# Kernel optimization log

Hardware: AMD Instinct MI355X
Metric: run time of the kernel (lower is better)

## Reference

```python
import jax, jax.numpy as jnp
import numpy as np

B, CIN, COUT = 16, 32, 64
T, H, W = 20, 32, 32
KT, KH, KW = 3, 3, 3
EPS = 1e-8
SURR_SCALE = 10.0  # SuperSpike surrogate slope


@jax.custom_vjp
def spike(x):
    # forward: heaviside; backward: SuperSpike surrogate gradient
    return (x > 0).astype(x.dtype)

def _spike_fwd(x):
    return (x > 0).astype(x.dtype), x

def _spike_bwd(x, g):
    return (g / (SURR_SCALE * jnp.abs(x) + 1.0) ** 2,)

spike.defvjp(_spike_fwd, _spike_bwd)


def _conv3d(x, w, pad, groups):
    return jax.lax.conv_general_dilated(
        x, w, window_strides=(1, 1, 1),
        padding=[(pad[0], pad[0]), (pad[1], pad[1]), (pad[2], pad[2])],
        rhs_dilation=(1, 1, 1),
        dimension_numbers=('NCDHW', 'OIDHW', 'NCDHW'),
        feature_group_count=groups)


def setup_inputs() -> dict:
    key = jax.random.key(0)
    k0, k1, k2 = jax.random.split(key, 3)
    w_init_mean, w_init_std = 0.05, 0.05
    w_mean = np.sqrt(w_init_mean)
    w_std = np.sqrt(np.sqrt(w_init_mean ** 2 + (w_init_std * np.sqrt(1.0 / (CIN * KT * KH * KW))) ** 2) - w_init_mean)
    x = jax.random.normal(k0, (B, CIN, T, H, W), dtype=jnp.float32)
    w_dw = w_mean + w_std * jax.random.normal(k1, (CIN, 1, KT, KH, KW), dtype=jnp.float32)
    w_pw = w_mean + w_std * jax.random.normal(k2, (COUT, CIN, 1, 1, 1), dtype=jnp.float32)
    beta = jnp.full((1,), 0.9, dtype=jnp.float32)  # one_per_layer, constant init, clamped [0,1]
    b = jnp.ones((COUT,), dtype=jnp.float32)       # constant init 1.0, clamped >= 0
    return {'x': x, 'w_dw': w_dw, 'w_pw': w_pw, 'beta': beta, 'b': b}


def reference(x, w_dw, w_pw, beta, b):
    pad = (1, 1, 1)  # ceil((3-1)*1/2) per dim; same padding also (faithfully) used for the 1x1x1 conv
    conv_x = _conv3d(x, w_dw, pad, CIN)[:, :, :, :H, :W]          # depthwise, crop to input_shape
    conv_x = _conv3d(conv_x, w_pw, pad, 1)[:, :, :, :H, :W]        # pointwise (time grows T -> T+2)
    nb_steps = conv_x.shape[2]

    # effective full kernel = depthwise * pointwise (broadcast over kernel dims)
    w_tmp = jnp.broadcast_to(jnp.transpose(w_dw, (1, 0, 2, 3, 4)), (COUT, CIN, KT, KH, KW)) * w_pw
    d = jnp.einsum('abcde,fbcde->af', w_tmp, w_tmp)                # lateral inhibition matrix [COUT, COUT]
    norm = (w_tmp ** 2).sum((1, 2, 3, 4))                          # [COUT]
    inv_norm = 1.0 / (norm + EPS)

    def step(carry, inp):
        mem, spk = carry
        rst = jnp.einsum('abcd,be->aecd', spk, d)                  # lateral reset
        mem = (mem - rst) * beta + inp * (1.0 - beta)              # leaky soft-reset update
        mthr = mem * inv_norm[None, :, None, None] - b[None, :, None, None]
        spk = spike(mthr)
        return (mem, spk), spk

    conv_t = jnp.moveaxis(conv_x, 2, 0)                            # [nb_steps, B, COUT, H, W]
    zeros = jnp.zeros((B, COUT, H, W), dtype=x.dtype)
    _, spks = jax.lax.scan(step, (zeros, zeros), conv_t)
    spk_rec = jnp.moveaxis(spks, 0, 2)                             # [B, COUT, nb_steps, H, W]

    loss = 0.5 * (spk_rec ** 2).mean()                             # 'squared'
    spk_spread_loss = spk_rec.sum((0, 1, 3, 4)).max() / (B * COUT * H * W)  # 'max'
    return spk_rec, loss, spk_spread_loss
```

## Files before the change

kernel.cpp:

```cpp
#include <hip/hip_runtime.h>

#define BB_   16
#define CIN_  32
#define COUT_ 64
#define TT_   20
#define NSTEP 22
#define NPIX  1024
#define HW_   32

typedef float f32x16 __attribute__((ext_vector_type(16)));

#define N_DWOUT 10485760ULL
#define N_DW2   10485760ULL
#define OFF_DWOUT 0ULL
#define OFF_DW2   (OFF_DWOUT + N_DWOUT)
#define OFF_D     (OFF_DW2 + N_DW2)
#define OFF_INVN  (OFF_D + 4096ULL)
#define OFF_CNT   (OFF_INVN + 64ULL)
#define WS_FLOATS (OFF_CNT + 32ULL)

__global__ __launch_bounds__(128)
void k_depthwise(const float* __restrict__ x, const float* __restrict__ wdw,
                 float* __restrict__ dwout) {
    const int blk = blockIdx.x;
    const int t4 = blk & 3;
    const int ci = (blk >> 2) & 31;
    const int b  = blk >> 7;
    const int tid = threadIdx.x;
    __shared__ float pl[3][34][35];

    float w[27];
#pragma unroll
    for (int k = 0; k < 27; ++k) w[k] = wdw[ci * 27 + k];

    for (int i = tid; i < 3 * 34 * 35; i += 128) (&pl[0][0][0])[i] = 0.f;
    __syncthreads();

    const float* xb = x + (size_t)(b * 32 + ci) * TT_ * NPIX;
    const int lr = tid >> 2;
    const int lc = (tid & 3) * 8;

    auto load_plane = [&](int p, int slot) {
        const float* s = xb + (size_t)p * NPIX + lr * 32 + lc;
        float4 v0 = *(const float4*)s;
        float4 v1 = *(const float4*)(s + 4);
        float* d = &pl[slot][1 + lr][1 + lc];
        d[0] = v0.x; d[1] = v0.y; d[2] = v0.z; d[3] = v0.w;
        d[4] = v1.x; d[5] = v1.y; d[6] = v1.z; d[7] = v1.w;
    };
    auto zero_plane = [&](int slot) {
        float* d = &pl[slot][1 + lr][1 + lc];
#pragma unroll
        for (int j = 0; j < 8; ++j) d[j] = 0.f;
    };

    const int T0 = t4 * 5;
    if (T0 > 0) load_plane(T0 - 1, (T0 - 1) % 3);
    load_plane(T0, T0 % 3);

    const int hd = lr, wd0 = lc;
    const float* base = &pl[0][0][0];

    for (int t = T0; t < T0 + 5; ++t) {
        __syncthreads();
        const int pnext = t + 1;
        if (pnext < TT_) load_plane(pnext, pnext % 3);
        else             zero_plane(pnext % 3);
        __syncthreads();

        const int sm1 = (t + 2) % 3, s0 = t % 3, sp1 = (t + 1) % 3;
        float acc[8] = {0.f,0.f,0.f,0.f,0.f,0.f,0.f,0.f};
#pragma unroll
        for (int kt = 0; kt < 3; ++kt) {
            const int slot = (kt == 0) ? sm1 : (kt == 1) ? s0 : sp1;
            const float* Pp = base + slot * (34 * 35);
#pragma unroll
            for (int kh = 0; kh < 3; ++kh) {
                const float* row = Pp + (hd + kh) * 35 + wd0;
                float r[10];
#pragma unroll
                for (int m = 0; m < 10; ++m) r[m] = row[m];
#pragma unroll
                for (int kw = 0; kw < 3; ++kw) {
                    const float wv = w[(kt * 3 + kh) * 3 + kw];
#pragma unroll
                    for (int j = 0; j < 8; ++j) acc[j] = fmaf(wv, r[j + kw], acc[j]);
                }
            }
        }
        float* dst = dwout + ((size_t)(b * 32 + ci) * TT_ + t) * NPIX + hd * 32 + wd0;
        *(float4*)dst       = make_float4(acc[0], acc[1], acc[2], acc[3]);
        *(float4*)(dst + 4) = make_float4(acc[4], acc[5], acc[6], acc[7]);
    }
}

__global__ __launch_bounds__(256)
void k_dmat(const float* __restrict__ wdw, const float* __restrict__ wpw,
            float* __restrict__ dmat, float* __restrict__ invn,
            unsigned* __restrict__ gcnt) {
    __shared__ double S[32];
    const int tid = threadIdx.x;
    if (tid < NSTEP) gcnt[tid] = 0u;
    if (tid < 32) {
        double s = 0.0;
        for (int k = 0; k < 27; ++k) { double v = (double)wdw[tid * 27 + k]; s += v * v; }
        S[tid] = s;
    }
    __syncthreads();
    for (int e = tid; e < 4096; e += 256) {
        const int a = e >> 6, f = e & 63;
        double acc = 0.0;
        for (int ci = 0; ci < 32; ++ci)
            acc += (double)wpw[a * 32 + ci] * (double)wpw[f * 32 + ci] * S[ci];
        dmat[e] = (float)acc;
        if (a == f) invn[a] = (float)(1.0 / (acc + 1e-8));
    }
}

__global__ __launch_bounds__(256)
void k_transpose(const float* __restrict__ dwout, float* __restrict__ dw2) {
    const int blk = blockIdx.x;
    const int hq = blk & 7;
    const int bt = blk >> 3;
    const int t  = bt % 20;
    const int b  = bt / 20;
    const int tid = threadIdx.x;
    __shared__ float lt[32][33];
    const int wsrc = tid & 31, cg = tid >> 5;

    for (int hh = 0; hh < 4; ++hh) {
        const int h = hq * 4 + hh;
#pragma unroll
        for (int cc = 0; cc < 4; ++cc) {
            const int ci = cc * 8 + cg;
            lt[wsrc][ci] = dwout[((size_t)(b * 32 + ci) * TT_ + t) * NPIX + h * 32 + wsrc];
        }
        __syncthreads();
        float* drow = dw2 + ((size_t)(b * TT_ + t) * 32 + h) * NPIX;
#pragma unroll
        for (int ss = 0; ss < 4; ++ss) {
            const int slot = ss * 8 + cg;
            drow[slot * 32 + wsrc] = (slot == 0) ? 0.f : lt[slot - 1][wsrc];
        }
        __syncthreads();
    }
}

__global__ __launch_bounds__(1024, 4)
void k_recur(const float* __restrict__ dw2, const float* __restrict__ wpw,
             const float* __restrict__ dmat, const float* __restrict__ invn_g,
             const float* __restrict__ beta_g, const float* __restrict__ bvec,
             float* __restrict__ out, unsigned* __restrict__ gcnt) {
    const int b = blockIdx.x >> 5, h = blockIdx.x & 31;
    const int tid = threadIdx.x;
    const int lane = tid & 63;
    const int co = lane;
    const int wid = __builtin_amdgcn_readfirstlane(tid >> 6);
    const int w0 = wid * 2;

    __shared__ float d_lds[4096];
    __shared__ unsigned long long msk[NSTEP][32];

    for (int i = tid; i < 4096; i += 1024) d_lds[i] = dmat[i];
    {
        unsigned long long* mp = &msk[0][0];
        for (int i = tid; i < NSTEP * 32; i += 1024) mp[i] = 0ull;
    }

    const float beta_v = beta_g[0];
    const float omb = 1.0f - beta_v;
    const float invn = invn_g[co];
    const float bth  = bvec[co];

    float wa[32];
#pragma unroll
    for (int ci = 0; ci < 32; ++ci) wa[ci] = wpw[co * 32 + ci];

    float mem0 = 0.f, mem1 = 0.f;
    unsigned long long m0p = 0ull, m1p = 0ull;

    __syncthreads();

    const int base0 = ((b * TT_) * 32 + (h - 1)) * NPIX + w0 * 32;
    const bool hok = (h >= 1);

    for (int t = 1; t < NSTEP; ++t) {
        float inp0 = 0.f, inp1 = 0.f;
        if (hok && t <= TT_) {
            const float* wrow = dw2 + (size_t)base0 + (size_t)(t - 1) * (32 * NPIX);
            const f32x16 A0 = *(const f32x16*)(wrow);
            const f32x16 A1 = *(const f32x16*)(wrow + 16);
            const f32x16 A2 = *(const f32x16*)(wrow + 32);
            const f32x16 A3 = *(const f32x16*)(wrow + 48);
#pragma unroll
            for (int ci = 0; ci < 16; ++ci) {
                inp0 = fmaf(wa[ci], A0[ci], inp0);
                inp1 = fmaf(wa[ci], A2[ci], inp1);
            }
#pragma unroll
            for (int ci = 0; ci < 16; ++ci) {
                inp0 = fmaf(wa[16 + ci], A1[ci], inp0);
                inp1 = fmaf(wa[16 + ci], A3[ci], inp1);
            }
        }
        float rst0 = 0.f, rst1 = 0.f;
        unsigned long long mm = m0p;
        while (mm) { const int a = __builtin_ctzll(mm); mm &= mm - 1; rst0 += d_lds[a * 64 + co]; }
        mm = m1p;
        while (mm) { const int a = __builtin_ctzll(mm); mm &= mm - 1; rst1 += d_lds[a * 64 + co]; }

        const float u0 = (mem0 - rst0) * beta_v;
        mem0 = u0 + inp0 * omb;
        const bool s0 = (mem0 * invn - bth) > 0.f;
        const float u1 = (mem1 - rst1) * beta_v;
        mem1 = u1 + inp1 * omb;
        const bool s1 = (mem1 * invn - bth) > 0.f;

        m0p = __ballot(s0);
        m1p = __ballot(s1);
        if (lane == 0) { msk[t][w0] = m0p; msk[t][w0 + 1] = m1p; }
    }
    __syncthreads();

    if (tid < NSTEP) {
        unsigned c = 0;
        for (int w = 0; w < 32; ++w) c += (unsigned)__popcll(msk[tid][w]);
        if (c) atomicAdd(&gcnt[tid], c);
    }

    const int wst = lane & 31;
    const int halfsel = lane >> 5;
    for (int it = 0; it < 44; ++it) {
        const int pair = it * 32 + wid * 2 + halfsel;
        const int tt = pair >> 6, cc = pair & 63;
        const unsigned long long wv = msk[tt][wst];
        const float sv = (float)((wv >> cc) & 1ull);
        out[((size_t)(b * 64 + cc) * NSTEP + tt) * NPIX + h * 32 + wst] = sv;
    }
}

__global__ void k_final(const unsigned* __restrict__ gcnt, float* __restrict__ out,
                        int out_size) {
    if (threadIdx.x == 0 && blockIdx.x == 0) {
        unsigned long long tot = 0; unsigned mx = 0;
        for (int t = 0; t < NSTEP; ++t) { const unsigned c = gcnt[t]; tot += c; if (c > mx) mx = c; }
        const long long nspk = (long long)out_size - 2;
        out[out_size - 2] = (float)(0.5 * ((double)tot / (double)nspk));
        out[out_size - 1] = (float)((double)mx / 1048576.0);
    }
}

extern "C" void kernel_launch(void* const* d_in, const int* in_sizes, int n_in,
                              void* d_out, int out_size, void* d_ws, size_t ws_size,
                              hipStream_t stream) {
    const float* x    = (const float*)d_in[0];
    const float* wdw  = (const float*)d_in[1];
    const float* wpw  = (const float*)d_in[2];
    const float* beta = (const float*)d_in[3];
    const float* bvec = (const float*)d_in[4];
    float* out = (float*)d_out;
    float* ws  = (float*)d_ws;

    if (ws_size < WS_FLOATS * sizeof(float)) return;

    float* dwout = ws + OFF_DWOUT;
    float* dw2   = ws + OFF_DW2;
    float* dmat  = ws + OFF_D;
    float* invn  = ws + OFF_INVN;
    unsigned* gcnt = (unsigned*)(ws + OFF_CNT);

    k_dmat     <<<1, 256, 0, stream>>>(wdw, wpw, dmat, invn, gcnt);
    k_depthwise<<<BB_ * CIN_ * 4, 128, 0, stream>>>(x, wdw, dwout);
    k_transpose<<<BB_ * TT_ * 8, 256, 0, stream>>>(dwout, dw2);
    k_recur    <<<BB_ * HW_, 1024, 0, stream>>>(dw2, wpw, dmat, invn, beta, bvec, out, gcnt);
    k_final    <<<1, 64, 0, stream>>>(gcnt, out, out_size);
}
```

Measured before the change: 99.39 us.

## Split recurrence blocks in half along width and prefetch next timestep inputs

The recurrence kernel now launches twice as many 512-thread blocks, each covering half the width of one row, so LDS mask storage and the output store loop are indexed per half. The dw2 loads for the next timestep are issued before the reset and spike update of the current step, so global memory latency overlaps with compute. Each block also writes zeros to the t=0 output slice for its half row, and the write loop covers timesteps 0 to 21. Each block still loads the full 4096-entry D matrix into LDS, so that load is now done twice as often.

```diff
diff --git a/kernel.cpp b/kernel.cpp
--- a/kernel.cpp
+++ b/kernel.cpp
@@ -146,25 +146,28 @@
     }
 }
 
-__global__ __launch_bounds__(1024, 4)
+__global__ __launch_bounds__(512)
 void k_recur(const float* __restrict__ dw2, const float* __restrict__ wpw,
              const float* __restrict__ dmat, const float* __restrict__ invn_g,
              const float* __restrict__ beta_g, const float* __restrict__ bvec,
              float* __restrict__ out, unsigned* __restrict__ gcnt) {
-    const int b = blockIdx.x >> 5, h = blockIdx.x & 31;
+    const int blk = blockIdx.x;
+    const int whalf = blk & 1;
+    const int h = (blk >> 1) & 31;
+    const int b = blk >> 6;
     const int tid = threadIdx.x;
     const int lane = tid & 63;
     const int co = lane;
     const int wid = __builtin_amdgcn_readfirstlane(tid >> 6);
-    const int w0 = wid * 2;
+    const int w0 = whalf * 16 + wid * 2;
 
     __shared__ float d_lds[4096];
-    __shared__ unsigned long long msk[NSTEP][32];
-
-    for (int i = tid; i < 4096; i += 1024) d_lds[i] = dmat[i];
+    __shared__ unsigned long long msk[NSTEP][16];
+
+    for (int i = tid; i < 4096; i += 512) d_lds[i] = dmat[i];
     {
         unsigned long long* mp = &msk[0][0];
-        for (int i = tid; i < NSTEP * 32; i += 1024) mp[i] = 0ull;
+        for (int i = tid; i < NSTEP * 16; i += 512) mp[i] = 0ull;
     }
 
     const float beta_v = beta_g[0];
@@ -179,19 +182,29 @@
     float mem0 = 0.f, mem1 = 0.f;
     unsigned long long m0p = 0ull, m1p = 0ull;
 
+    {
+        const int zco = tid >> 3, zw = (tid & 7) * 2;
+        *(float2*)(out + ((size_t)(b * 64 + zco) * NSTEP) * NPIX + h * 32 + whalf * 16 + zw)
+            = make_float2(0.f, 0.f);
+    }
+
     __syncthreads();
 
     const int base0 = ((b * TT_) * 32 + (h - 1)) * NPIX + w0 * 32;
     const bool hok = (h >= 1);
+
+    f32x16 A0, A1, A2, A3;
+    if (hok) {
+        const float* wrow = dw2 + (size_t)base0;
+        A0 = *(const f32x16*)(wrow);
+        A1 = *(const f32x16*)(wrow + 16);
+        A2 = *(const f32x16*)(wrow + 32);
+        A3 = *(const f32x16*)(wrow + 48);
+    }
 
     for (int t = 1; t < NSTEP; ++t) {
         float inp0 = 0.f, inp1 = 0.f;
         if (hok && t <= TT_) {
-            const float* wrow = dw2 + (size_t)base0 + (size_t)(t - 1) * (32 * NPIX);
-            const f32x16 A0 = *(const f32x16*)(wrow);
-            const f32x16 A1 = *(const f32x16*)(wrow + 16);
-            const f32x16 A2 = *(const f32x16*)(wrow + 32);
-            const f32x16 A3 = *(const f32x16*)(wrow + 48);
 #pragma unroll
             for (int ci = 0; ci < 16; ++ci) {
                 inp0 = fmaf(wa[ci], A0[ci], inp0);
@@ -203,6 +216,14 @@
                 inp1 = fmaf(wa[16 + ci], A3[ci], inp1);
             }
         }
+        if (hok && t < TT_) {
+            const float* wrow = dw2 + (size_t)base0 + (size_t)t * (32 * NPIX);
+            A0 = *(const f32x16*)(wrow);
+            A1 = *(const f32x16*)(wrow + 16);
+            A2 = *(const f32x16*)(wrow + 32);
+            A3 = *(const f32x16*)(wrow + 48);
+        }
+
         float rst0 = 0.f, rst1 = 0.f;
         unsigned long long mm = m0p;
         while (mm) { const int a = __builtin_ctzll(mm); mm &= mm - 1; rst0 += d_lds[a * 64 + co]; }
@@ -218,24 +239,24 @@
 
         m0p = __ballot(s0);
         m1p = __ballot(s1);
-        if (lane == 0) { msk[t][w0] = m0p; msk[t][w0 + 1] = m1p; }
+        const int wl = wid * 2;
+        if (lane == 0) { msk[t][wl] = m0p; msk[t][wl + 1] = m1p; }
     }
     __syncthreads();
 
     if (tid < NSTEP) {
         unsigned c = 0;
-        for (int w = 0; w < 32; ++w) c += (unsigned)__popcll(msk[tid][w]);
+        for (int w = 0; w < 16; ++w) c += (unsigned)__popcll(msk[tid][w]);
         if (c) atomicAdd(&gcnt[tid], c);
     }
 
-    const int wst = lane & 31;
-    const int halfsel = lane >> 5;
+    const int wl = tid & 15;
     for (int it = 0; it < 44; ++it) {
-        const int pair = it * 32 + wid * 2 + halfsel;
-        const int tt = pair >> 6, cc = pair & 63;
-        const unsigned long long wv = msk[tt][wst];
+        const int r = it * 32 + (tid >> 4);
+        const int tt = r >> 6, cc = r & 63;
+        const unsigned long long wv = msk[tt][wl];
         const float sv = (float)((wv >> cc) & 1ull);
-        out[((size_t)(b * 64 + cc) * NSTEP + tt) * NPIX + h * 32 + wst] = sv;
+        out[((size_t)(b * 64 + cc) * NSTEP + tt) * NPIX + h * 32 + whalf * 16 + wl] = sv;
     }
 }
 
@@ -272,6 +293,6 @@
     k_dmat     <<<1, 256, 0, stream>>>(wdw, wpw, dmat, invn, gcnt);
     k_depthwise<<<BB_ * CIN_ * 4, 128, 0, stream>>>(x, wdw, dwout);
     k_transpose<<<BB_ * TT_ * 8, 256, 0, stream>>>(dwout, dw2);
-    k_recur    <<<BB_ * HW_, 1024, 0, stream>>>(dw2, wpw, dmat, invn, beta, bvec, out, gcnt);
+    k_recur    <<<BB_ * HW_ * 2, 512, 0, stream>>>(dw2, wpw, dmat, invn, beta, bvec, out, gcnt);
     k_final    <<<1, 64, 0, stream>>>(gcnt, out, out_size);
 }
```

After: 89.72 us. 9.7% less time.
